# Kernel optimization log

Measured on AMD Instinct MI355X. Metric: run time of the kernel, lower is better.

The kernel has to match this reference:

```python
import jax, jax.numpy as jnp
import numpy as np

NEG_SLOPE = 0.2  # LeakyReLU slope

def setup_inputs() -> dict:
    key = jax.random.key(0)
    k1, k2, k3, k4, k5 = jax.random.split(key, 5)
    H, hidden, code_dim, n_codes = 4, 256, 512, 200000
    return {
        "provider_emb": jax.random.normal(k1, (1, code_dim), dtype=jnp.float32),
        "code_embs": jax.random.normal(k2, (n_codes, code_dim), dtype=jnp.float32),
        "Ws": jax.random.normal(k3, (H, hidden, code_dim), dtype=jnp.float32) * 0.05,
        "bs": jax.random.normal(k4, (H, hidden), dtype=jnp.float32) * 0.05,
        "a_s": jax.random.normal(k5, (H, 2 * hidden), dtype=jnp.float32),
    }

def reference(provider_emb, code_embs, Ws, bs, a_s):
    # Ws: [H, hidden, code_dim], bs: [H, hidden], a_s: [H, 2*hidden]
    hidden = Ws.shape[1]
    a1 = a_s[:, :hidden]   # applied to provider part  [H, hidden]
    a2 = a_s[:, hidden:]   # applied to code part      [H, hidden]
    # provider_h: [H, hidden]
    provider_h = jnp.einsum('hdc,c->hd', Ws, provider_emb[0]) + bs
    # code_h: [H, n, hidden]
    code_h = jnp.einsum('hdc,nc->hnd', Ws, code_embs) + bs[:, None, :]
    # e_i = leaky_relu(provider_h . a1 + code_h_i . a2)  -> [H, n]
    p_score = jnp.einsum('hd,hd->h', provider_h, a1)            # [H]
    c_score = jnp.einsum('hnd,hd->hn', code_h, a2)              # [H, n]
    e = p_score[:, None] + c_score
    e = jnp.where(e >= 0, e, NEG_SLOPE * e)                     # leaky_relu(0.2)
    alpha = jax.nn.softmax(e, axis=1)                           # softmax over codes (dim 0 in torch)
    return alpha  # [num_heads, n_codes]
```

## Files before the change

### kernel.cpp

```cpp
#include <hip/hip_runtime.h>
#include <hip/hip_bf16.h>

#define H     4
#define HID   256
#define CDIM  512
#define NCH   32
#define DPER  (HID / NCH)
#define NB    2048

typedef float f32x4 __attribute__((ext_vector_type(4)));

#define WS_P1   0
#define WS_P2   (WS_P1 + H * NCH * CDIM)
#define WS_W2   (WS_P2 + H * NCH * CDIM)
#define WS_PRE  (WS_W2 + H * CDIM)
#define WS_GMAX (WS_PRE + H)
#define WS_GINV (WS_GMAX + H)
#define WS_BMS  (WS_GINV + H)

__global__ void __launch_bounds__(256) prepA_kernel(
    const float* __restrict__ Ws, const float* __restrict__ as_,
    float* __restrict__ ws)
{
    int h = blockIdx.x >> 5, chunk = blockIdx.x & (NCH - 1);
    int t = threadIdx.x;
    const float* W  = Ws + ((size_t)h * HID + chunk * DPER) * CDIM;
    const float* a1 = as_ + (size_t)h * 2 * HID + chunk * DPER;
    const float* a2 = a1 + HID;
    int c0 = t, c1 = t + 256;
    float w1a = 0.f, w1b = 0.f, w2a = 0.f, w2b = 0.f;
#pragma unroll
    for (int d = 0; d < DPER; ++d) {
        float x0 = W[d * CDIM + c0], x1 = W[d * CDIM + c1];
        float v1 = a1[d], v2 = a2[d];
        w1a = fmaf(v1, x0, w1a); w2a = fmaf(v2, x0, w2a);
        w1b = fmaf(v1, x1, w1b); w2b = fmaf(v2, x1, w2b);
    }
    size_t base = (size_t)(h * NCH + chunk) * CDIM;
    ws[WS_P1 + base + c0] = w1a; ws[WS_P1 + base + c1] = w1b;
    ws[WS_P2 + base + c0] = w2a; ws[WS_P2 + base + c1] = w2b;
}

__global__ void __launch_bounds__(256) prepB_kernel(
    const float* __restrict__ pe, const float* __restrict__ bs,
    const float* __restrict__ as_, float* __restrict__ ws)
{
    int h = blockIdx.x;
    int t = threadIdx.x;
    int c0 = t, c1 = t + 256;
    float w1a = 0.f, w1b = 0.f, w2a = 0.f, w2b = 0.f;
#pragma unroll
    for (int k = 0; k < NCH; ++k) {
        size_t base = (size_t)(h * NCH + k) * CDIM;
        w1a += ws[WS_P1 + base + c0]; w1b += ws[WS_P1 + base + c1];
        w2a += ws[WS_P2 + base + c0]; w2b += ws[WS_P2 + base + c1];
    }
    ws[WS_W2 + h * CDIM + c0] = w2a;
    ws[WS_W2 + h * CDIM + c1] = w2b;
    const float* a1 = as_ + (size_t)h * 2 * HID;
    const float* a2 = a1 + HID;
    float contrib = w1a * pe[c0] + w1b * pe[c1];
    contrib += bs[h * HID + t] * (a1[t] + a2[t]);
    __shared__ float red[256];
    red[t] = contrib;
    __syncthreads();
    for (int s2 = 128; s2 > 0; s2 >>= 1) {
        if (t < s2) red[t] += red[t + s2];
        __syncthreads();
    }
    if (t == 0) ws[WS_PRE + h] = red[0];
}

__global__ void __launch_bounds__(256) score_kernel(
    const float* __restrict__ codes, const float* __restrict__ ws_in,
    float* __restrict__ e_out, float* __restrict__ ws_out, int n_codes)
{
    const int lane = threadIdx.x & 63;
    const int wid  = threadIdx.x >> 6;
    const int gw   = blockIdx.x * 4 + wid;
    const long long Wtot = (long long)gridDim.x * 4;

    f32x4 w2a[H], w2b[H];
#pragma unroll
    for (int h = 0; h < H; ++h) {
        w2a[h] = *(const f32x4*)&ws_in[WS_W2 + h * CDIM + 4 * lane];
        w2b[h] = *(const f32x4*)&ws_in[WS_W2 + h * CDIM + 256 + 4 * lane];
    }
    const int  hsel = lane & 3;
    const bool b0 = lane & 1, b1 = lane & 2, b2 = lane & 4;
    const float mypre = ws_in[WS_PRE + hsel];

    const long long npairs = (long long)n_codes >> 1;
    const long long ps = (long long)gw * npairs / Wtot;
    const long long pe_ = ((long long)gw + 1) * npairs / Wtot;

    float m = -1e30f, s = 0.f;

    for (long long p = ps; p < pe_; ++p) {
        const f32x4* r = (const f32x4*)(codes + ((size_t)p << 1) * CDIM);
        f32x4 xa0 = __builtin_nontemporal_load(&r[lane]);
        f32x4 xb0 = __builtin_nontemporal_load(&r[64 + lane]);
        f32x4 xa1 = __builtin_nontemporal_load(&r[128 + lane]);
        f32x4 xb1 = __builtin_nontemporal_load(&r[192 + lane]);

        float A0[H], A1[H];
#pragma unroll
        for (int h = 0; h < H; ++h) {
            A0[h] = xa0.x * w2a[h].x + xa0.y * w2a[h].y +
                    xa0.z * w2a[h].z + xa0.w * w2a[h].w +
                    xb0.x * w2b[h].x + xb0.y * w2b[h].y +
                    xb0.z * w2b[h].z + xb0.w * w2b[h].w;
            A1[h] = xa1.x * w2a[h].x + xa1.y * w2a[h].y +
                    xa1.z * w2a[h].z + xa1.w * w2a[h].w +
                    xb1.x * w2b[h].x + xb1.y * w2b[h].y +
                    xb1.z * w2b[h].z + xb1.w * w2b[h].w;
        }
#pragma unroll
        for (int h = 0; h < H; ++h) {
            A0[h] += __shfl_xor(A0[h], 1, 64);
            A0[h] += __shfl_xor(A0[h], 2, 64);
            A1[h] += __shfl_xor(A1[h], 1, 64);
            A1[h] += __shfl_xor(A1[h], 2, 64);
        }
        float t01 = b0 ? A0[1] : A0[0], t23 = b0 ? A0[3] : A0[2];
        float B0 = b1 ? t23 : t01;
        t01 = b0 ? A1[1] : A1[0]; t23 = b0 ? A1[3] : A1[2];
        float B1 = b1 ? t23 : t01;
        B0 += __shfl_xor(B0, 4, 64);
        B1 += __shfl_xor(B1, 4, 64);
        float C = b2 ? B1 : B0;
        C += __shfl_xor(C, 8, 64);
        C += __shfl_xor(C, 16, 64);
        C += __shfl_xor(C, 32, 64);

        float e = mypre + C;
        e = e >= 0.f ? e : 0.2f * e;
        float mm = fmaxf(m, e);
        s = s * __expf(m - mm) + __expf(e - mm);
        m = mm;
        if (!(lane & 56)) {
            e_out[(size_t)hsel * n_codes + ((size_t)p << 1) + (b2 ? 1 : 0)] = e;
        }
    }

    if ((n_codes & 1) && gw == Wtot - 1) {
        const int n0 = n_codes - 1;
        const f32x4* r = (const f32x4*)(codes + (size_t)n0 * CDIM);
        f32x4 xa = __builtin_nontemporal_load(&r[lane]);
        f32x4 xb = __builtin_nontemporal_load(&r[64 + lane]);
        float A[H];
#pragma unroll
        for (int h = 0; h < H; ++h) {
            A[h] = xa.x * w2a[h].x + xa.y * w2a[h].y +
                   xa.z * w2a[h].z + xa.w * w2a[h].w +
                   xb.x * w2b[h].x + xb.y * w2b[h].y +
                   xb.z * w2b[h].z + xb.w * w2b[h].w;
            A[h] += __shfl_xor(A[h], 1, 64);
            A[h] += __shfl_xor(A[h], 2, 64);
        }
        float t01 = b0 ? A[1] : A[0], t23 = b0 ? A[3] : A[2];
        float v = b1 ? t23 : t01;
#pragma unroll
        for (int msk = 4; msk <= 32; msk <<= 1) v += __shfl_xor(v, msk, 64);
        float e = mypre + v;
        e = e >= 0.f ? e : 0.2f * e;
        if (!b2) {
            float mm = fmaxf(m, e);
            s = s * __expf(m - mm) + __expf(e - mm);
            m = mm;
        }
        if (lane < H) e_out[(size_t)hsel * n_codes + n0] = e;
    }

    {
        float M2 = __shfl_xor(m, 4, 64);
        float S2 = __shfl_xor(s, 4, 64);
        float mm = fmaxf(m, M2);
        s = s * __expf(m - mm) + S2 * __expf(M2 - mm);
        m = mm;
    }

    __shared__ float lm[4][H], ls[4][H];
    if (lane < H) { lm[wid][lane] = m; ls[wid][lane] = s; }
    __syncthreads();
    if (threadIdx.x < H) {
        int h = threadIdx.x;
        float M = -1e30f, S = 0.f;
#pragma unroll
        for (int w = 0; w < 4; ++w) {
            float mm = fmaxf(M, lm[w][h]);
            S = S * __expf(M - mm) + ls[w][h] * __expf(lm[w][h] - mm);
            M = mm;
        }
        float2 v = make_float2(M, S);
        *(float2*)&ws_out[WS_BMS + (size_t)(h * NB + blockIdx.x) * 2] = v;
    }
}

__global__ void __launch_bounds__(256) sreduce_kernel(float* __restrict__ ws)
{
    int lane = threadIdx.x & 63;
    int h    = threadIdx.x >> 6;
    float M = -1e30f, S = 0.f;
    for (int i = lane; i < NB; i += 64) {
        float2 v = *(const float2*)&ws[WS_BMS + (size_t)(h * NB + i) * 2];
        float mm = fmaxf(M, v.x);
        S = S * __expf(M - mm) + v.y * __expf(v.x - mm);
        M = mm;
    }
    for (int msk = 32; msk; msk >>= 1) {
        float M2 = __shfl_xor(M, msk, 64);
        float S2 = __shfl_xor(S, msk, 64);
        float mm = fmaxf(M, M2);
        S = S * __expf(M - mm) + S2 * __expf(M2 - mm);
        M = mm;
    }
    if (lane == 0) { ws[WS_GMAX + h] = M; ws[WS_GINV + h] = 1.f / S; }
}

__global__ void __launch_bounds__(256) norm_kernel(
    float* __restrict__ e, const float* __restrict__ ws, int n_codes)
{
    int i = blockIdx.x * blockDim.x + threadIdx.x;
    int perh = n_codes >> 2;
    int tot = H * perh;
    if (i >= tot) return;
    int h = i / perh;
    float gm = ws[WS_GMAX + h], gi = ws[WS_GINV + h];
    float4 v = ((float4*)e)[i];
    v.x = __expf(v.x - gm) * gi;
    v.y = __expf(v.y - gm) * gi;
    v.z = __expf(v.z - gm) * gi;
    v.w = __expf(v.w - gm) * gi;
    ((float4*)e)[i] = v;
}

extern "C" void kernel_launch(void* const* d_in, const int* in_sizes, int n_in,
                              void* d_out, int out_size, void* d_ws, size_t ws_size,
                              hipStream_t stream)
{
    const float* pe    = (const float*)d_in[0];
    const float* codes = (const float*)d_in[1];
    const float* Ws    = (const float*)d_in[2];
    const float* bs    = (const float*)d_in[3];
    const float* as_   = (const float*)d_in[4];
    float* out = (float*)d_out;
    float* ws  = (float*)d_ws;
    int n_codes = in_sizes[1] / CDIM;

    prepA_kernel<<<H * NCH, 256, 0, stream>>>(Ws, as_, ws);
    prepB_kernel<<<H, 256, 0, stream>>>(pe, bs, as_, ws);
    score_kernel<<<NB, 256, 0, stream>>>(codes, ws, out, ws, n_codes);
    sreduce_kernel<<<1, 256, 0, stream>>>(ws);
    int tot4 = (H * n_codes) / 4;
    norm_kernel<<<(tot4 + 255) / 256, 256, 0, stream>>>(out, ws, n_codes);
}
```

Baseline: 98.41 us.

## Process four codes per wave with double-buffered loads and fuse softmax reduce into normalize

The score kernel now handles four code rows per wave iteration, not two. It double-buffers register loads so the next quad's loads are issued before the current quad is computed, aiming to hide memory latency on the 400MB stream of code embeddings. The separate single-block sreduce kernel is removed: each normalize block redundantly reduces the 2048 per-block (max, sum) partials for its head, which saves a launch and a serialization point at the cost of duplicated reduction work. Register pressure rises from holding two quads of loaded data.

New measurement: 88.62 us. 9.9% less time.

```diff
diff --git a/kernel.cpp b/kernel.cpp
--- a/kernel.cpp
+++ b/kernel.cpp
@@ -14,9 +14,7 @@
 #define WS_P2   (WS_P1 + H * NCH * CDIM)
 #define WS_W2   (WS_P2 + H * NCH * CDIM)
 #define WS_PRE  (WS_W2 + H * CDIM)
-#define WS_GMAX (WS_PRE + H)
-#define WS_GINV (WS_GMAX + H)
-#define WS_BMS  (WS_GINV + H)
+#define WS_BMS  (WS_PRE + H)
 
 __global__ void __launch_bounds__(256) prepA_kernel(
     const float* __restrict__ Ws, const float* __restrict__ as_,
@@ -71,6 +69,73 @@
     if (t == 0) ws[WS_PRE + h] = red[0];
 }
 
+__device__ __forceinline__ void load_quad(const float* __restrict__ codes,
+                                          long long q, int lane, f32x4 v[8])
+{
+    const f32x4* R = (const f32x4*)codes + ((size_t)q << 9);
+#pragma unroll
+    for (int r = 0; r < 4; ++r) {
+        v[2 * r]     = __builtin_nontemporal_load(R + r * 128 + lane);
+        v[2 * r + 1] = __builtin_nontemporal_load(R + r * 128 + 64 + lane);
+    }
+}
+
+__device__ __forceinline__ void online_merge(float& m, float& s, float m2, float s2)
+{
+    float mm = fmaxf(m, m2);
+    s = s * __expf(m - mm) + s2 * __expf(m2 - mm);
+    m = mm;
+}
+
+__device__ __forceinline__ void compute_quad(
+    const f32x4 v[8], const f32x4 w2a[H], const f32x4 w2b[H],
+    float mypre, int lane, int hsel, bool b0, bool b1, bool b2, bool b3,
+    long long q, int n_codes, float* __restrict__ e_out, float& m, float& s)
+{
+    float A[4][H];
+#pragma unroll
+    for (int r = 0; r < 4; ++r)
+#pragma unroll
+        for (int h = 0; h < H; ++h) {
+            A[r][h] = v[2*r].x * w2a[h].x + v[2*r].y * w2a[h].y +
+                      v[2*r].z * w2a[h].z + v[2*r].w * w2a[h].w +
+                      v[2*r+1].x * w2b[h].x + v[2*r+1].y * w2b[h].y +
+                      v[2*r+1].z * w2b[h].z + v[2*r+1].w * w2b[h].w;
+        }
+#pragma unroll
+    for (int r = 0; r < 4; ++r)
+#pragma unroll
+        for (int h = 0; h < H; ++h) {
+            A[r][h] += __shfl_xor(A[r][h], 1, 64);
+            A[r][h] += __shfl_xor(A[r][h], 2, 64);
+        }
+    float B[4];
+#pragma unroll
+    for (int r = 0; r < 4; ++r) {
+        float t01 = b0 ? A[r][1] : A[r][0];
+        float t23 = b0 ? A[r][3] : A[r][2];
+        B[r] = b1 ? t23 : t01;
+        B[r] += __shfl_xor(B[r], 4, 64);
+    }
+    float C0 = b2 ? B[1] : B[0];
+    float C1 = b2 ? B[3] : B[2];
+    C0 += __shfl_xor(C0, 8, 64);
+    C1 += __shfl_xor(C1, 8, 64);
+    float z = b3 ? C1 : C0;
+    z += __shfl_xor(z, 16, 64);
+    z += __shfl_xor(z, 32, 64);
+
+    float e = mypre + z;
+    e = e >= 0.f ? e : 0.2f * e;
+    float mm = fmaxf(m, e);
+    s = s * __expf(m - mm) + __expf(e - mm);
+    m = mm;
+    if (!(lane & 48)) {
+        int rowslot = (lane >> 2) & 3;
+        e_out[(size_t)hsel * n_codes + ((size_t)q << 2) + rowslot] = e;
+    }
+}
+
 __global__ void __launch_bounds__(256) score_kernel(
     const float* __restrict__ codes, const float* __restrict__ ws_in,
     float* __restrict__ e_out, float* __restrict__ ws_out, int n_codes)
@@ -87,97 +152,66 @@
         w2b[h] = *(const f32x4*)&ws_in[WS_W2 + h * CDIM + 256 + 4 * lane];
     }
     const int  hsel = lane & 3;
-    const bool b0 = lane & 1, b1 = lane & 2, b2 = lane & 4;
+    const bool b0 = lane & 1, b1 = lane & 2, b2 = lane & 4, b3 = lane & 8;
     const float mypre = ws_in[WS_PRE + hsel];
 
-    const long long npairs = (long long)n_codes >> 1;
-    const long long ps = (long long)gw * npairs / Wtot;
-    const long long pe_ = ((long long)gw + 1) * npairs / Wtot;
+    const long long nquads = (long long)n_codes >> 2;
+    const long long qs = (long long)gw * nquads / Wtot;
+    const long long qe = ((long long)gw + 1) * nquads / Wtot;
 
     float m = -1e30f, s = 0.f;
 
-    for (long long p = ps; p < pe_; ++p) {
-        const f32x4* r = (const f32x4*)(codes + ((size_t)p << 1) * CDIM);
-        f32x4 xa0 = __builtin_nontemporal_load(&r[lane]);
-        f32x4 xb0 = __builtin_nontemporal_load(&r[64 + lane]);
-        f32x4 xa1 = __builtin_nontemporal_load(&r[128 + lane]);
-        f32x4 xb1 = __builtin_nontemporal_load(&r[192 + lane]);
-
-        float A0[H], A1[H];
-#pragma unroll
-        for (int h = 0; h < H; ++h) {
-            A0[h] = xa0.x * w2a[h].x + xa0.y * w2a[h].y +
-                    xa0.z * w2a[h].z + xa0.w * w2a[h].w +
-                    xb0.x * w2b[h].x + xb0.y * w2b[h].y +
-                    xb0.z * w2b[h].z + xb0.w * w2b[h].w;
-            A1[h] = xa1.x * w2a[h].x + xa1.y * w2a[h].y +
-                    xa1.z * w2a[h].z + xa1.w * w2a[h].w +
-                    xb1.x * w2b[h].x + xb1.y * w2b[h].y +
-                    xb1.z * w2b[h].z + xb1.w * w2b[h].w;
+    f32x4 P[8], Q[8];
+    long long q = qs;
+    if (q < qe) load_quad(codes, q, lane, P);
+    while (q + 2 <= qe) {
+        load_quad(codes, q + 1, lane, Q);
+        compute_quad(P, w2a, w2b, mypre, lane, hsel, b0, b1, b2, b3,
+                     q, n_codes, e_out, m, s);
+        if (q + 2 < qe) load_quad(codes, q + 2, lane, P);
+        compute_quad(Q, w2a, w2b, mypre, lane, hsel, b0, b1, b2, b3,
+                     q + 1, n_codes, e_out, m, s);
+        q += 2;
+    }
+    if (q < qe)
+        compute_quad(P, w2a, w2b, mypre, lane, hsel, b0, b1, b2, b3,
+                     q, n_codes, e_out, m, s);
+
+    if (gw == Wtot - 1) {
+        for (int n0 = (int)(nquads << 2); n0 < n_codes; ++n0) {
+            const f32x4* R = (const f32x4*)codes + (size_t)n0 * 128;
+            f32x4 xa = __builtin_nontemporal_load(R + lane);
+            f32x4 xb = __builtin_nontemporal_load(R + 64 + lane);
+            float A[H];
+#pragma unroll
+            for (int h = 0; h < H; ++h) {
+                A[h] = xa.x * w2a[h].x + xa.y * w2a[h].y +
+                       xa.z * w2a[h].z + xa.w * w2a[h].w +
+                       xb.x * w2b[h].x + xb.y * w2b[h].y +
+                       xb.z * w2b[h].z + xb.w * w2b[h].w;
+                A[h] += __shfl_xor(A[h], 1, 64);
+                A[h] += __shfl_xor(A[h], 2, 64);
+            }
+            float t01 = b0 ? A[1] : A[0], t23 = b0 ? A[3] : A[2];
+            float v = b1 ? t23 : t01;
+#pragma unroll
+            for (int msk = 4; msk <= 32; msk <<= 1) v += __shfl_xor(v, msk, 64);
+            float e = mypre + v;
+            e = e >= 0.f ? e : 0.2f * e;
+            if (!(lane & 12)) {
+                float mm = fmaxf(m, e);
+                s = s * __expf(m - mm) + __expf(e - mm);
+                m = mm;
+            }
+            if (lane < H) e_out[(size_t)hsel * n_codes + n0] = e;
         }
-#pragma unroll
-        for (int h = 0; h < H; ++h) {
-            A0[h] += __shfl_xor(A0[h], 1, 64);
-            A0[h] += __shfl_xor(A0[h], 2, 64);
-            A1[h] += __shfl_xor(A1[h], 1, 64);
-            A1[h] += __shfl_xor(A1[h], 2, 64);
-        }
-        float t01 = b0 ? A0[1] : A0[0], t23 = b0 ? A0[3] : A0[2];
-        float B0 = b1 ? t23 : t01;
-        t01 = b0 ? A1[1] : A1[0]; t23 = b0 ? A1[3] : A1[2];
-        float B1 = b1 ? t23 : t01;
-        B0 += __shfl_xor(B0, 4, 64);
-        B1 += __shfl_xor(B1, 4, 64);
-        float C = b2 ? B1 : B0;
-        C += __shfl_xor(C, 8, 64);
-        C += __shfl_xor(C, 16, 64);
-        C += __shfl_xor(C, 32, 64);
-
-        float e = mypre + C;
-        e = e >= 0.f ? e : 0.2f * e;
-        float mm = fmaxf(m, e);
-        s = s * __expf(m - mm) + __expf(e - mm);
-        m = mm;
-        if (!(lane & 56)) {
-            e_out[(size_t)hsel * n_codes + ((size_t)p << 1) + (b2 ? 1 : 0)] = e;
-        }
-    }
-
-    if ((n_codes & 1) && gw == Wtot - 1) {
-        const int n0 = n_codes - 1;
-        const f32x4* r = (const f32x4*)(codes + (size_t)n0 * CDIM);
-        f32x4 xa = __builtin_nontemporal_load(&r[lane]);
-        f32x4 xb = __builtin_nontemporal_load(&r[64 + lane]);
-        float A[H];
-#pragma unroll
-        for (int h = 0; h < H; ++h) {
-            A[h] = xa.x * w2a[h].x + xa.y * w2a[h].y +
-                   xa.z * w2a[h].z + xa.w * w2a[h].w +
-                   xb.x * w2b[h].x + xb.y * w2b[h].y +
-                   xb.z * w2b[h].z + xb.w * w2b[h].w;
-            A[h] += __shfl_xor(A[h], 1, 64);
-            A[h] += __shfl_xor(A[h], 2, 64);
-        }
-        float t01 = b0 ? A[1] : A[0], t23 = b0 ? A[3] : A[2];
-        float v = b1 ? t23 : t01;
-#pragma unroll
-        for (int msk = 4; msk <= 32; msk <<= 1) v += __shfl_xor(v, msk, 64);
-        float e = mypre + v;
-        e = e >= 0.f ? e : 0.2f * e;
-        if (!b2) {
-            float mm = fmaxf(m, e);
-            s = s * __expf(m - mm) + __expf(e - mm);
-            m = mm;
-        }
-        if (lane < H) e_out[(size_t)hsel * n_codes + n0] = e;
     }
 
     {
-        float M2 = __shfl_xor(m, 4, 64);
-        float S2 = __shfl_xor(s, 4, 64);
-        float mm = fmaxf(m, M2);
-        s = s * __expf(m - mm) + S2 * __expf(M2 - mm);
-        m = mm;
+        float M2 = __shfl_xor(m, 4, 64), S2 = __shfl_xor(s, 4, 64);
+        online_merge(m, s, M2, S2);
+        M2 = __shfl_xor(m, 8, 64); S2 = __shfl_xor(s, 8, 64);
+        online_merge(m, s, M2, S2);
     }
 
     __shared__ float lm[4][H], ls[4][H];
@@ -187,52 +221,54 @@
         int h = threadIdx.x;
         float M = -1e30f, S = 0.f;
 #pragma unroll
-        for (int w = 0; w < 4; ++w) {
-            float mm = fmaxf(M, lm[w][h]);
-            S = S * __expf(M - mm) + ls[w][h] * __expf(lm[w][h] - mm);
-            M = mm;
-        }
+        for (int w = 0; w < 4; ++w) online_merge(M, S, lm[w][h], ls[w][h]);
         float2 v = make_float2(M, S);
         *(float2*)&ws_out[WS_BMS + (size_t)(h * NB + blockIdx.x) * 2] = v;
     }
 }
 
-__global__ void __launch_bounds__(256) sreduce_kernel(float* __restrict__ ws)
-{
-    int lane = threadIdx.x & 63;
-    int h    = threadIdx.x >> 6;
-    float M = -1e30f, S = 0.f;
-    for (int i = lane; i < NB; i += 64) {
-        float2 v = *(const float2*)&ws[WS_BMS + (size_t)(h * NB + i) * 2];
-        float mm = fmaxf(M, v.x);
-        S = S * __expf(M - mm) + v.y * __expf(v.x - mm);
-        M = mm;
-    }
-    for (int msk = 32; msk; msk >>= 1) {
-        float M2 = __shfl_xor(M, msk, 64);
-        float S2 = __shfl_xor(S, msk, 64);
-        float mm = fmaxf(M, M2);
-        S = S * __expf(M - mm) + S2 * __expf(M2 - mm);
-        M = mm;
-    }
-    if (lane == 0) { ws[WS_GMAX + h] = M; ws[WS_GINV + h] = 1.f / S; }
-}
-
 __global__ void __launch_bounds__(256) norm_kernel(
     float* __restrict__ e, const float* __restrict__ ws, int n_codes)
 {
-    int i = blockIdx.x * blockDim.x + threadIdx.x;
-    int perh = n_codes >> 2;
-    int tot = H * perh;
-    if (i >= tot) return;
-    int h = i / perh;
-    float gm = ws[WS_GMAX + h], gi = ws[WS_GINV + h];
-    float4 v = ((float4*)e)[i];
-    v.x = __expf(v.x - gm) * gi;
-    v.y = __expf(v.y - gm) * gi;
-    v.z = __expf(v.z - gm) * gi;
-    v.w = __expf(v.w - gm) * gi;
-    ((float4*)e)[i] = v;
+    const int h    = blockIdx.y;
+    const int lane = threadIdx.x & 63;
+    const int wid  = threadIdx.x >> 6;
+
+    float M = -1e30f, S = 0.f;
+    const float* Pp = &ws[WS_BMS + (size_t)h * NB * 2];
+    for (int i = threadIdx.x; i < NB; i += 256) {
+        float2 v = *(const float2*)&Pp[2 * i];
+        online_merge(M, S, v.x, v.y);
+    }
+#pragma unroll
+    for (int msk = 1; msk < 64; msk <<= 1) {
+        float M2 = __shfl_xor(M, msk, 64), S2 = __shfl_xor(S, msk, 64);
+        online_merge(M, S, M2, S2);
+    }
+    __shared__ float sm[4], ss[4];
+    if (lane == 0) { sm[wid] = M; ss[wid] = S; }
+    __syncthreads();
+    float gm = -1e30f, gs = 0.f;
+#pragma unroll
+    for (int w = 0; w < 4; ++w) online_merge(gm, gs, sm[w], ss[w]);
+    float gi = 1.f / gs;
+
+    int perh4 = n_codes >> 2;
+    int idx = blockIdx.x * 256 + threadIdx.x;
+    if (idx < perh4) {
+        float4* ep = (float4*)(e + (size_t)h * n_codes) + idx;
+        float4 v = *ep;
+        v.x = __expf(v.x - gm) * gi;
+        v.y = __expf(v.y - gm) * gi;
+        v.z = __expf(v.z - gm) * gi;
+        v.w = __expf(v.w - gm) * gi;
+        *ep = v;
+    }
+    if (blockIdx.x == 0 && threadIdx.x < (n_codes & 3)) {
+        int n0 = (perh4 << 2) + threadIdx.x;
+        float x = e[(size_t)h * n_codes + n0];
+        e[(size_t)h * n_codes + n0] = __expf(x - gm) * gi;
+    }
 }
 
 extern "C" void kernel_launch(void* const* d_in, const int* in_sizes, int n_in,
@@ -251,7 +287,7 @@
     prepA_kernel<<<H * NCH, 256, 0, stream>>>(Ws, as_, ws);
     prepB_kernel<<<H, 256, 0, stream>>>(pe, bs, as_, ws);
     score_kernel<<<NB, 256, 0, stream>>>(codes, ws, out, ws, n_codes);
-    sreduce_kernel<<<1, 256, 0, stream>>>(ws);
-    int tot4 = (H * n_codes) / 4;
-    norm_kernel<<<(tot4 + 255) / 256, 256, 0, stream>>>(out, ws, n_codes);
-}
+    int perh4 = n_codes >> 2;
+    dim3 ngrid((perh4 + 255) / 256, H);
+    norm_kernel<<<ngrid, 256, 0, stream>>>(out, ws, n_codes);
+}
```
